# Optimization experiments

Measured on AMD Instinct MI355X. Metric: run time of the kernel, lower is better.

## Reference

```python
import jax, jax.numpy as jnp
import numpy as np

B, C, H, W, MODES, RANK = 16, 128, 128, 128, 16, 8


def setup_inputs() -> dict:
    key = jax.random.key(0)
    ks = jax.random.split(key, 8)
    scale = 1.0 / (C * C)
    lr_scale = 0.02
    return {
        "x": jax.random.normal(ks[0], (B, C, H, W), dtype=jnp.float32),
        "w_real": scale * jax.random.normal(ks[1], (C, C, MODES, MODES), dtype=jnp.float32),
        "w_imag": scale * jax.random.normal(ks[2], (C, C, MODES, MODES), dtype=jnp.float32),
        "u_real": lr_scale * jax.random.normal(ks[3], (C, RANK, MODES, MODES), dtype=jnp.float32),
        "u_imag": lr_scale * jax.random.normal(ks[4], (C, RANK, MODES, MODES), dtype=jnp.float32),
        "v_real": lr_scale * jax.random.normal(ks[5], (C, RANK, MODES, MODES), dtype=jnp.float32),
        "v_imag": lr_scale * jax.random.normal(ks[6], (C, RANK, MODES, MODES), dtype=jnp.float32),
        "skip_w": (1.0 / np.sqrt(C)) * jax.random.normal(ks[7], (C, C), dtype=jnp.float32),
    }


def physical_act(x):
    # f(x) = x * exp(-|x|^2)
    return x * jnp.exp(-jnp.abs(x) ** 2)


def reference(x, w_real, w_imag, u_real, u_imag, v_real, v_imag, skip_w):
    Bb, Cc, Hh, Ww = x.shape
    # 1x1 conv skip path == channel matmul
    x_skip = jnp.einsum('oc,bchw->bohw', skip_w, x)
    # FFT to spectral domain: (B, C, H, W//2+1) complex64
    x_ft = jnp.fft.rfft2(x, norm='ortho')
    W_ft = x_ft.shape[-1]
    m1 = min(w_real.shape[-2], Hh)
    m2 = min(w_real.shape[-1], W_ft)
    # truncated-mode complex diagonal operator D (per-frequency channel mix)
    D = (w_real + 1j * w_imag)[:, :, :m1, :m2]          # (O, I, m1, m2)
    x_top = x_ft[:, :, :m1, :m2]                         # (B, I, m1, m2)
    out_top = jnp.einsum('bimn,oimn->bomn', x_top, D)
    # low-rank cross-frequency mixer UV*
    U = (u_real + 1j * u_imag)[:, :, :m1, :m2]           # (O, R, m1, m2)
    V = (v_real + 1j * v_imag)[:, :, :m1, :m2]           # (I, R, m1, m2)
    z = jnp.einsum('bimn,irmn->br', x_top, jnp.conj(V))  # (B, R)
    out_top = out_top + jnp.einsum('ormn,br->bomn', U, z)
    # scatter back into zero-padded full spectrum
    out_ft = jnp.zeros(x_ft.shape, dtype=x_ft.dtype).at[:, :, :m1, :m2].set(out_top)
    x_spectral = jnp.fft.irfft2(out_ft, s=(Hh, Ww), norm='ortho')
    out = x_spectral + x_skip
    return physical_act(out)
```

## Files before the change

kernel.cpp:

```cpp
#include <hip/hip_runtime.h>
#include <math.h>

#define TAB_OFF 0
#define XTOP_OFF 16384
#define Z_OFF (16384 + 1048576)
#define OTOP_OFF (Z_OFF + 256)


using bf16x8 = __attribute__((ext_vector_type(8))) short;
using s16x4  = __attribute__((ext_vector_type(4))) short;
using f32x16 = __attribute__((ext_vector_type(16))) float;

__device__ inline unsigned short bf_rnd(float v) {
  return (unsigned short)((__float_as_uint(v) + 0x8000u) >> 16);
}
__device__ inline void bf_split(float v, unsigned short& hi, unsigned short& lo) {
  unsigned u = __float_as_uint(v);
  hi = (unsigned short)(u >> 16);
  float r = v - __uint_as_float(u & 0xFFFF0000u);
  lo = (unsigned short)(__float_as_uint(r) >> 16);
}
__device__ inline bf16x8 ldfrag(const unsigned short* p) {
  s16x4 a = *(const s16x4*)p;
  s16x4 b = *(const s16x4*)(p + 4);
  bf16x8 r;
  r[0] = a[0]; r[1] = a[1]; r[2] = a[2]; r[3] = a[3];
  r[4] = b[0]; r[5] = b[1]; r[6] = b[2]; r[7] = b[3];
  return r;
}

__global__ __launch_bounds__(256) void k_tab(float* __restrict__ tab) {
  int idx = blockIdx.x * 256 + threadIdx.x;
  if (idx >= 16384) return;
  int which = idx >> 11, rem = idx & 2047;
  int a, j;
  if (which == 4 || which == 5) { a = rem & 127; j = rem >> 7; }
  else { a = rem >> 4; j = rem & 15; }
  int p = (a * j) & 127;
  float ang = (float)p * (float)(3.14159265358979323846 / 64.0);
  float cv = cosf(ang), sv = sinf(ang);
  float v;
  switch (which) {
    case 0: v = cv * (1.f / 128.f); break;
    case 1: v = -sv * (1.f / 128.f); break;
    case 2: v = cv; break;
    case 3: v = sv; break;
    case 4: v = cv; break;
    case 5: v = sv; break;
    case 6: v = ((rem & 15) == 0 ? 1.f : 2.f) * cv * (1.f / 128.f); break;
    default: v = ((rem & 15) == 0 ? 1.f : 2.f) * (-sv) * (1.f / 128.f); break;
  }
  tab[idx] = v;
}

__global__ __launch_bounds__(128) void k_fwd(const float* __restrict__ x,
                                             const float* __restrict__ tab,
                                             float* __restrict__ xtop) {
  __shared__ float Ar[16][132];
  __shared__ float Ai[16][132];
  const int c = blockIdx.x, b = blockIdx.y;
  const int t = threadIdx.x;
  const float* row = x + (((size_t)(b * 128 + c)) << 14) + (size_t)t * 128;

  float ar[16], ai[16];
  #pragma unroll
  for (int n = 0; n < 16; ++n) { ar[n] = 0.f; ai[n] = 0.f; }

  for (int w0 = 0; w0 < 128; w0 += 16) {
    float xv[16];
    #pragma unroll
    for (int q = 0; q < 4; ++q)
      *(float4*)&xv[q * 4] = *(const float4*)(row + w0 + q * 4);
    #pragma unroll
    for (int w = 0; w < 16; ++w) {
      const float* tc = tab + (w0 + w) * 16;
      const float* ts = tab + 2048 + (w0 + w) * 16;
      #pragma unroll
      for (int n = 0; n < 16; ++n) {
        ar[n] += xv[w] * tc[n];
        ai[n] += xv[w] * ts[n];
      }
    }
  }
  #pragma unroll
  for (int n = 0; n < 16; ++n) { Ar[n][t] = ar[n]; Ai[n][t] = ai[n]; }
  __syncthreads();

  const int n = t & 15, m0 = t >> 4;
  const float* tc0 = tab + 8192 + m0 * 128;
  const float* ts0 = tab + 10240 + m0 * 128;
  const float* tc1 = tc0 + 1024;
  const float* ts1 = ts0 + 1024;
  float xr0 = 0.f, xi0 = 0.f, xr1 = 0.f, xi1 = 0.f;
  for (int h4 = 0; h4 < 128; h4 += 4) {
    float arv[4], aiv[4], cc0[4], ss0[4], cc1[4], ss1[4];
    *(float4*)arv = *(const float4*)&Ar[n][h4];
    *(float4*)aiv = *(const float4*)&Ai[n][h4];
    *(float4*)cc0 = *(const float4*)(tc0 + h4);
    *(float4*)ss0 = *(const float4*)(ts0 + h4);
    *(float4*)cc1 = *(const float4*)(tc1 + h4);
    *(float4*)ss1 = *(const float4*)(ts1 + h4);
    #pragma unroll
    for (int j = 0; j < 4; ++j) {
      xr0 += arv[j] * cc0[j] + aiv[j] * ss0[j];
      xi0 += aiv[j] * cc0[j] - arv[j] * ss0[j];
      xr1 += arv[j] * cc1[j] + aiv[j] * ss1[j];
      xi1 += aiv[j] * cc1[j] - arv[j] * ss1[j];
    }
  }
  size_t base = ((size_t)(b * 128 + c)) * 512 + (size_t)t * 2;
  xtop[base] = xr0; xtop[base + 1] = xi0;
  xtop[base + 256] = xr1; xtop[base + 257] = xi1;
}

__global__ __launch_bounds__(256) void k_z(const float* __restrict__ xtop,
                                           const float* __restrict__ vre,
                                           const float* __restrict__ vim,
                                           float* __restrict__ zout) {
  int b = blockIdx.x, ic = blockIdx.y, t = threadIdx.x;
  float zr[8], zi[8];
  #pragma unroll
  for (int r = 0; r < 8; ++r) { zr[r] = 0.f; zi[r] = 0.f; }
  const float* xb = xtop + ((size_t)b * 128) * 512;
  for (int i = ic * 16; i < ic * 16 + 16; ++i) {
    float xr = xb[i * 512 + t * 2], xi = xb[i * 512 + t * 2 + 1];
    #pragma unroll
    for (int r = 0; r < 8; ++r) {
      float vr = vre[(size_t)(i * 8 + r) * 256 + t];
      float vi = vim[(size_t)(i * 8 + r) * 256 + t];
      zr[r] += xr * vr + xi * vi;
      zi[r] += xi * vr - xr * vi;
    }
  }
  #pragma unroll
  for (int r = 0; r < 8; ++r)
    for (int off = 32; off > 0; off >>= 1) {
      zr[r] += __shfl_down(zr[r], off);
      zi[r] += __shfl_down(zi[r], off);
    }
  __shared__ float red[4][16];
  int wid = t >> 6, lane = t & 63;
  if (lane == 0) {
    #pragma unroll
    for (int r = 0; r < 8; ++r) { red[wid][r * 2] = zr[r]; red[wid][r * 2 + 1] = zi[r]; }
  }
  __syncthreads();
  if (t < 16) atomicAdd(&zout[b * 16 + t], red[0][t] + red[1][t] + red[2][t] + red[3][t]);
}

__global__ __launch_bounds__(256) void k_mix(const float* __restrict__ xtop,
                                             const float* __restrict__ wre,
                                             const float* __restrict__ wim,
                                             const float* __restrict__ ure,
                                             const float* __restrict__ uim,
                                             const float* __restrict__ z,
                                             float* __restrict__ otop) {
  int o0 = blockIdx.x * 4, b0 = blockIdx.y * 2, ic = blockIdx.z, t = threadIdx.x;
  float ar[2][4], ai[2][4];
  #pragma unroll
  for (int bb = 0; bb < 2; ++bb)
    #pragma unroll
    for (int oo = 0; oo < 4; ++oo) { ar[bb][oo] = 0.f; ai[bb][oo] = 0.f; }
  const float* x0 = xtop + ((size_t)(b0 * 128)) * 512;
  const float* x1 = x0 + 128 * 512;
  for (int i = ic * 16; i < ic * 16 + 16; ++i) {
    float x0r = x0[i * 512 + t * 2], x0i = x0[i * 512 + t * 2 + 1];
    float x1r = x1[i * 512 + t * 2], x1i = x1[i * 512 + t * 2 + 1];
    #pragma unroll
    for (int oo = 0; oo < 4; ++oo) {
      size_t di = (size_t)((o0 + oo) * 128 + i) * 256 + t;
      float dr = wre[di], dj = wim[di];
      ar[0][oo] += dr * x0r - dj * x0i; ai[0][oo] += dr * x0i + dj * x0r;
      ar[1][oo] += dr * x1r - dj * x1i; ai[1][oo] += dr * x1i + dj * x1r;
    }
  }
  if (ic == 0) {
    float zr[2][8], zi[2][8];
    #pragma unroll
    for (int bb = 0; bb < 2; ++bb)
      #pragma unroll
      for (int r = 0; r < 8; ++r) {
        zr[bb][r] = z[(b0 + bb) * 16 + r * 2];
        zi[bb][r] = z[(b0 + bb) * 16 + r * 2 + 1];
      }
    #pragma unroll
    for (int oo = 0; oo < 4; ++oo)
      #pragma unroll
      for (int r = 0; r < 8; ++r) {
        float urv = ure[(size_t)((o0 + oo) * 8 + r) * 256 + t];
        float uiv = uim[(size_t)((o0 + oo) * 8 + r) * 256 + t];
        #pragma unroll
        for (int bb = 0; bb < 2; ++bb) {
          ar[bb][oo] += urv * zr[bb][r] - uiv * zi[bb][r];
          ai[bb][oo] += urv * zi[bb][r] + uiv * zr[bb][r];
        }
      }
  }
  #pragma unroll
  for (int bb = 0; bb < 2; ++bb)
    #pragma unroll
    for (int oo = 0; oo < 4; ++oo) {
      size_t oi = ((size_t)((b0 + bb) * 128 + o0 + oo) * 256 + (size_t)t) * 2;
      atomicAdd(&otop[oi], ar[bb][oo]);
      atomicAdd(&otop[oi + 1], ai[bb][oo]);
    }
}

__global__ __launch_bounds__(256) void k_out(const float* __restrict__ x,
                                             const float* __restrict__ sw,
                                             const float* __restrict__ otop,
                                             const float* __restrict__ tab,
                                             float* __restrict__ out) {
  __shared__ unsigned short Ylds[128 * 36];
  __shared__ unsigned short Tlds[128 * 36];
  __shared__ unsigned short Bh[128 * 36], Bl[128 * 36];
  __shared__ unsigned short Ah[128 * 36], Al[128 * 36];
  const int h = blockIdx.x, b = blockIdx.y;
  const int t = threadIdx.x;
  const int lane = t & 63, wv = t >> 6;

  {
    int w = t >> 1, half = t & 1;
    const float* src = tab + (half ? 14336 : 12288) + w * 16;
    #pragma unroll
    for (int q = 0; q < 4; ++q) {
      float4 v = *(const float4*)(src + q * 4);
      int k0 = half * 16 + q * 4;
      Tlds[w * 36 + k0 + 0] = bf_rnd(v.x);
      Tlds[w * 36 + k0 + 1] = bf_rnd(v.y);
      Tlds[w * 36 + k0 + 2] = bf_rnd(v.z);
      Tlds[w * 36 + k0 + 3] = bf_rnd(v.w);
    }
  }
  {
    int o = t >> 1, nh = (t & 1) * 8;
    float yr[8], yi[8];
    #pragma unroll
    for (int j = 0; j < 8; ++j) { yr[j] = 0.f; yi[j] = 0.f; }
    const float* xb = otop + ((size_t)(b * 128 + o)) * 512 + nh * 2;
    #pragma unroll 4
    for (int m = 0; m < 16; ++m) {
      float cm = tab[4096 + h * 16 + m];
      float sm = tab[6144 + h * 16 + m];
      float4 q0 = *(const float4*)(xb + m * 32 + 0);
      float4 q1 = *(const float4*)(xb + m * 32 + 4);
      float4 q2 = *(const float4*)(xb + m * 32 + 8);
      float4 q3 = *(const float4*)(xb + m * 32 + 12);
      yr[0] += q0.x * cm - q0.y * sm; yi[0] += q0.x * sm + q0.y * cm;
      yr[1] += q0.z * cm - q0.w * sm; yi[1] += q0.z * sm + q0.w * cm;
      yr[2] += q1.x * cm - q1.y * sm; yi[2] += q1.x * sm + q1.y * cm;
      yr[3] += q1.z * cm - q1.w * sm; yi[3] += q1.z * sm + q1.w * cm;
      yr[4] += q2.x * cm - q2.y * sm; yi[4] += q2.x * sm + q2.y * cm;
      yr[5] += q2.z * cm - q2.w * sm; yi[5] += q2.z * sm + q2.w * cm;
      yr[6] += q3.x * cm - q3.y * sm; yi[6] += q3.x * sm + q3.y * cm;
      yr[7] += q3.z * cm - q3.w * sm; yi[7] += q3.z * sm + q3.w * cm;
    }
    #pragma unroll
    for (int j = 0; j < 8; ++j) {
      Ylds[o * 36 + nh + j] = bf_rnd(yr[j]);
      Ylds[o * 36 + 16 + nh + j] = bf_rnd(yi[j]);
    }
  }
  __syncthreads();

  f32x16 acc[4];
  #pragma unroll
  for (int nt = 0; nt < 4; ++nt)
    #pragma unroll
    for (int e = 0; e < 16; ++e) acc[nt][e] = 0.f;

  for (int kc = 0; kc < 4; ++kc) {
    float xv[16], wv16[16];
    #pragma unroll
    for (int it = 0; it < 16; ++it) {
      int c = kc * 32 + it * 2 + (t >> 7);
      int w = t & 127;
      xv[it] = x[(size_t)(b * 128 + c) * 16384 + (size_t)h * 128 + w];
    }
    #pragma unroll
    for (int it = 0; it < 16; ++it) {
      int idx = it * 256 + t;
      int o = idx >> 5, cl = idx & 31;
      wv16[it] = sw[o * 128 + kc * 32 + cl];
    }
    __syncthreads();
    #pragma unroll
    for (int it = 0; it < 16; ++it) {
      int cl = it * 2 + (t >> 7);
      int w = t & 127;
      unsigned short hb, lb;
      bf_split(xv[it], hb, lb);
      Bh[w * 36 + cl] = hb; Bl[w * 36 + cl] = lb;
    }
    #pragma unroll
    for (int it = 0; it < 16; ++it) {
      int idx = it * 256 + t;
      int o = idx >> 5, cl = idx & 31;
      unsigned short hb, lb;
      bf_split(wv16[it], hb, lb);
      Ah[o * 36 + cl] = hb; Al[o * 36 + cl] = lb;
    }
    __syncthreads();
    #pragma unroll
    for (int ks = 0; ks < 2; ++ks) {
      const int kb = ks * 16 + (lane >> 5) * 8;
      bf16x8 ah = ldfrag(&Ah[(wv * 32 + (lane & 31)) * 36 + kb]);
      bf16x8 al = ldfrag(&Al[(wv * 32 + (lane & 31)) * 36 + kb]);
      #pragma unroll
      for (int nt = 0; nt < 4; ++nt) {
        bf16x8 bh_ = ldfrag(&Bh[(nt * 32 + (lane & 31)) * 36 + kb]);
        bf16x8 bl_ = ldfrag(&Bl[(nt * 32 + (lane & 31)) * 36 + kb]);
        acc[nt] = __builtin_amdgcn_mfma_f32_32x32x16_bf16(ah, bh_, acc[nt], 0, 0, 0);
        acc[nt] = __builtin_amdgcn_mfma_f32_32x32x16_bf16(ah, bl_, acc[nt], 0, 0, 0);
        acc[nt] = __builtin_amdgcn_mfma_f32_32x32x16_bf16(al, bh_, acc[nt], 0, 0, 0);
      }
    }
  }

  #pragma unroll
  for (int ks = 0; ks < 2; ++ks) {
    const int kb = ks * 16 + (lane >> 5) * 8;
    bf16x8 ya = ldfrag(&Ylds[(wv * 32 + (lane & 31)) * 36 + kb]);
    #pragma unroll
    for (int nt = 0; nt < 4; ++nt) {
      bf16x8 tb = ldfrag(&Tlds[(nt * 32 + (lane & 31)) * 36 + kb]);
      acc[nt] = __builtin_amdgcn_mfma_f32_32x32x16_bf16(ya, tb, acc[nt], 0, 0, 0);
    }
  }

  #pragma unroll
  for (int nt = 0; nt < 4; ++nt) {
    int w = nt * 32 + (lane & 31);
    #pragma unroll
    for (int r = 0; r < 16; ++r) {
      int o = wv * 32 + (r & 3) + 8 * (r >> 2) + 4 * (lane >> 5);
      float v = acc[nt][r];
      out[((size_t)(b * 128 + o)) * 16384 + (size_t)h * 128 + w] = v * __expf(-v * v);
    }
  }
}

extern "C" void kernel_launch(void* const* d_in, const int* in_sizes, int n_in,
                              void* d_out, int out_size, void* d_ws, size_t ws_size,
                              hipStream_t stream) {
  const float* x  = (const float*)d_in[0];
  const float* wr = (const float*)d_in[1];
  const float* wi = (const float*)d_in[2];
  const float* ur = (const float*)d_in[3];
  const float* ui = (const float*)d_in[4];
  const float* vr = (const float*)d_in[5];
  const float* vi = (const float*)d_in[6];
  const float* sw = (const float*)d_in[7];
  float* out  = (float*)d_out;
  float* ws   = (float*)d_ws;
  float* tab  = ws + TAB_OFF;
  float* xtop = ws + XTOP_OFF;
  float* z    = ws + Z_OFF;
  float* otop = ws + OTOP_OFF;

  hipMemsetAsync(z, 0, 256 * sizeof(float), stream);
  hipMemsetAsync(otop, 0, 1048576 * sizeof(float), stream);
  hipLaunchKernelGGL(k_tab, dim3(64), dim3(256), 0, stream, tab);
  hipLaunchKernelGGL(k_fwd, dim3(128, 16), dim3(128), 0, stream, x, tab, xtop);
  hipLaunchKernelGGL(k_z,   dim3(16, 8), dim3(256), 0, stream, xtop, vr, vi, z);
  hipLaunchKernelGGL(k_mix, dim3(32, 8, 8), dim3(256), 0, stream, xtop, wr, wi, ur, ui, z, otop);
  hipLaunchKernelGGL(k_out, dim3(128, 16), dim3(256), 0, stream, x, sw, otop, tab, out);
}
```

Baseline: 219.0 us.

## Compute forward W-direction DFT with bf16 MFMA and split-precision twiddles

The first DFT stage of k_fwd, 128 rows by 16 frequencies for both cosine and sine, moves from scalar FP32 FMAs to 32x32x16 bf16 MFMA instructions. The input image is rounded to bf16 in swizzled LDS. The twiddle table is split into hi/lo bf16 parts by a new prep kernel to keep twiddle accuracy. The block grows to 256 threads, and the second H-direction stage now gives each thread one output instead of two. This removes a compute-heavy scalar loop, at the cost of bf16 rounding of x, which could hurt accuracy, plus an extra small launch.

```diff
diff --git a/kernel.cpp b/kernel.cpp
--- a/kernel.cpp
+++ b/kernel.cpp
@@ -5,6 +5,7 @@
 #define XTOP_OFF 16384
 #define Z_OFF (16384 + 1048576)
 #define OTOP_OFF (Z_OFF + 256)
+#define TF_OFF (OTOP_OFF + 1048576)
 
 
 using bf16x8 = __attribute__((ext_vector_type(8))) short;
@@ -27,6 +28,10 @@
   r[0] = a[0]; r[1] = a[1]; r[2] = a[2]; r[3] = a[3];
   r[4] = b[0]; r[5] = b[1]; r[6] = b[2]; r[7] = b[3];
   return r;
+}
+__device__ inline bf16x8 ldfrag_sw(const unsigned short* base, int row, int koff) {
+  int byte = row * 256 + ((koff * 2) ^ ((row & 7) << 4));
+  return ldfrag((const unsigned short*)((const char*)base + byte));
 }
 
 __global__ __launch_bounds__(256) void k_tab(float* __restrict__ tab) {
@@ -53,64 +58,104 @@
   tab[idx] = v;
 }
 
-__global__ __launch_bounds__(128) void k_fwd(const float* __restrict__ x,
+__global__ __launch_bounds__(256) void k_fprep(unsigned short* __restrict__ tf) {
+  int idx = blockIdx.x * 256 + threadIdx.x;
+  if (idx >= 4096) return;
+  int np = idx >> 7, k = idx & 127;
+  int n = np & 15;
+  int p = (k * n) & 127;
+  float ang = (float)p * (float)(3.14159265358979323846 / 64.0);
+  float v = (np < 16 ? cosf(ang) : -sinf(ang)) * (1.f / 128.f);
+  unsigned short hi, lo;
+  bf_split(v, hi, lo);
+  tf[np * 128 + k] = hi;
+  tf[4096 + np * 128 + k] = lo;
+}
+
+__global__ __launch_bounds__(256) void k_fwd(const float* __restrict__ x,
+                                             const unsigned short* __restrict__ tf,
                                              const float* __restrict__ tab,
                                              float* __restrict__ xtop) {
-  __shared__ float Ar[16][132];
-  __shared__ float Ai[16][132];
+  __shared__ unsigned short Xh[128 * 128];
+  __shared__ unsigned short Tfh[32 * 128];
+  __shared__ unsigned short Tfl[32 * 128];
   const int c = blockIdx.x, b = blockIdx.y;
   const int t = threadIdx.x;
-  const float* row = x + (((size_t)(b * 128 + c)) << 14) + (size_t)t * 128;
-
-  float ar[16], ai[16];
-  #pragma unroll
-  for (int n = 0; n < 16; ++n) { ar[n] = 0.f; ai[n] = 0.f; }
-
-  for (int w0 = 0; w0 < 128; w0 += 16) {
-    float xv[16];
-    #pragma unroll
-    for (int q = 0; q < 4; ++q)
-      *(float4*)&xv[q * 4] = *(const float4*)(row + w0 + q * 4);
-    #pragma unroll
-    for (int w = 0; w < 16; ++w) {
-      const float* tc = tab + (w0 + w) * 16;
-      const float* ts = tab + 2048 + (w0 + w) * 16;
-      #pragma unroll
-      for (int n = 0; n < 16; ++n) {
-        ar[n] += xv[w] * tc[n];
-        ai[n] += xv[w] * ts[n];
-      }
-    }
-  }
-  #pragma unroll
-  for (int n = 0; n < 16; ++n) { Ar[n][t] = ar[n]; Ai[n][t] = ai[n]; }
+  const int lane = t & 63, wv = t >> 6;
+
+  #pragma unroll
+  for (int it = 0; it < 32; ++it) {
+    int idx = it * 256 + t;
+    int part = idx >> 12, rem = idx & 4095;
+    int row = rem >> 7, k = rem & 127;
+    unsigned short v = tf[part * 4096 + rem];
+    unsigned short* dst = part ? Tfl : Tfh;
+    *(unsigned short*)((char*)dst + row * 256 + ((k * 2) ^ ((row & 7) << 4))) = v;
+  }
+  const float* img = x + (((size_t)(b * 128 + c)) << 14);
+  #pragma unroll
+  for (int it = 0; it < 16; ++it) {
+    int flat = it * 256 + t;
+    int h = flat >> 5, wq = flat & 31;
+    float4 v = *(const float4*)(img + (size_t)flat * 4);
+    s16x4 pk;
+    pk[0] = (short)bf_rnd(v.x); pk[1] = (short)bf_rnd(v.y);
+    pk[2] = (short)bf_rnd(v.z); pk[3] = (short)bf_rnd(v.w);
+    *(s16x4*)((char*)Xh + h * 256 + ((wq * 8) ^ ((h & 7) << 4))) = pk;
+  }
   __syncthreads();
 
-  const int n = t & 15, m0 = t >> 4;
-  const float* tc0 = tab + 8192 + m0 * 128;
-  const float* ts0 = tab + 10240 + m0 * 128;
-  const float* tc1 = tc0 + 1024;
-  const float* ts1 = ts0 + 1024;
-  float xr0 = 0.f, xi0 = 0.f, xr1 = 0.f, xi1 = 0.f;
-  for (int h4 = 0; h4 < 128; h4 += 4) {
-    float arv[4], aiv[4], cc0[4], ss0[4], cc1[4], ss1[4];
-    *(float4*)arv = *(const float4*)&Ar[n][h4];
-    *(float4*)aiv = *(const float4*)&Ai[n][h4];
-    *(float4*)cc0 = *(const float4*)(tc0 + h4);
-    *(float4*)ss0 = *(const float4*)(ts0 + h4);
-    *(float4*)cc1 = *(const float4*)(tc1 + h4);
-    *(float4*)ss1 = *(const float4*)(ts1 + h4);
-    #pragma unroll
-    for (int j = 0; j < 4; ++j) {
-      xr0 += arv[j] * cc0[j] + aiv[j] * ss0[j];
-      xi0 += aiv[j] * cc0[j] - arv[j] * ss0[j];
-      xr1 += arv[j] * cc1[j] + aiv[j] * ss1[j];
-      xi1 += aiv[j] * cc1[j] - arv[j] * ss1[j];
-    }
-  }
-  size_t base = ((size_t)(b * 128 + c)) * 512 + (size_t)t * 2;
-  xtop[base] = xr0; xtop[base + 1] = xi0;
-  xtop[base + 256] = xr1; xtop[base + 257] = xi1;
+  f32x16 acc;
+  #pragma unroll
+  for (int e = 0; e < 16; ++e) acc[e] = 0.f;
+  const int orow = wv * 32 + (lane & 31);
+  const int bcol = lane & 31;
+  const int kh8 = (lane >> 5) * 8;
+  #pragma unroll
+  for (int kc8 = 0; kc8 < 8; ++kc8) {
+    int kfull = kc8 * 16 + kh8;
+    bf16x8 a  = ldfrag_sw(Xh, orow, kfull);
+    bf16x8 th = ldfrag_sw(Tfh, bcol, kfull);
+    bf16x8 tl = ldfrag_sw(Tfl, bcol, kfull);
+    acc = __builtin_amdgcn_mfma_f32_32x32x16_bf16(a, th, acc, 0, 0, 0);
+    acc = __builtin_amdgcn_mfma_f32_32x32x16_bf16(a, tl, acc, 0, 0, 0);
+  }
+  __syncthreads();
+
+  float* Arp = (float*)Xh;
+  float* Aip = Arp + 16 * 132;
+  {
+    const int col = lane & 31;
+    #pragma unroll
+    for (int r = 0; r < 16; ++r) {
+      int h = wv * 32 + (r & 3) + 8 * (r >> 2) + 4 * (lane >> 5);
+      if (col < 16) Arp[col * 132 + h] = acc[r];
+      else          Aip[(col - 16) * 132 + h] = acc[r];
+    }
+  }
+  __syncthreads();
+
+  {
+    const int m = t >> 4, n = t & 15;
+    const float* tc = tab + 8192 + m * 128;
+    const float* ts = tab + 10240 + m * 128;
+    const float* ar = Arp + n * 132;
+    const float* ai = Aip + n * 132;
+    float xr = 0.f, xi = 0.f;
+    #pragma unroll 8
+    for (int h4 = 0; h4 < 128; h4 += 4) {
+      float4 av = *(const float4*)(ar + h4);
+      float4 iv = *(const float4*)(ai + h4);
+      float4 cv = *(const float4*)(tc + h4);
+      float4 sv = *(const float4*)(ts + h4);
+      xr += av.x * cv.x + iv.x * sv.x;  xi += iv.x * cv.x - av.x * sv.x;
+      xr += av.y * cv.y + iv.y * sv.y;  xi += iv.y * cv.y - av.y * sv.y;
+      xr += av.z * cv.z + iv.z * sv.z;  xi += iv.z * cv.z - av.z * sv.z;
+      xr += av.w * cv.w + iv.w * sv.w;  xi += iv.w * cv.w - av.w * sv.w;
+    }
+    size_t base = ((size_t)(b * 128 + c)) * 512 + (size_t)(m * 16 + n) * 2;
+    xtop[base] = xr; xtop[base + 1] = xi;
+  }
 }
 
 __global__ __launch_bounds__(256) void k_z(const float* __restrict__ xtop,
@@ -357,11 +402,13 @@
   float* xtop = ws + XTOP_OFF;
   float* z    = ws + Z_OFF;
   float* otop = ws + OTOP_OFF;
+  unsigned short* tf = (unsigned short*)(ws + TF_OFF);
 
   hipMemsetAsync(z, 0, 256 * sizeof(float), stream);
   hipMemsetAsync(otop, 0, 1048576 * sizeof(float), stream);
   hipLaunchKernelGGL(k_tab, dim3(64), dim3(256), 0, stream, tab);
-  hipLaunchKernelGGL(k_fwd, dim3(128, 16), dim3(128), 0, stream, x, tab, xtop);
+  hipLaunchKernelGGL(k_fprep, dim3(16), dim3(256), 0, stream, tf);
+  hipLaunchKernelGGL(k_fwd, dim3(128, 16), dim3(256), 0, stream, x, tf, tab, xtop);
   hipLaunchKernelGGL(k_z,   dim3(16, 8), dim3(256), 0, stream, xtop, vr, vi, z);
   hipLaunchKernelGGL(k_mix, dim3(32, 8, 8), dim3(256), 0, stream, xtop, wr, wi, ur, ui, z, otop);
   hipLaunchKernelGGL(k_out, dim3(128, 16), dim3(256), 0, stream, x, sw, otop, tab, out);
```

Result: faster. 207.3 us (-5.4%).
